# Optimization experiments

Measured on AMD Instinct MI355X. Metric: run time of the kernel, lower is better.

Reference implementation:

```python
import jax, jax.numpy as jnp
import numpy as np

B, C, H, W = 16, 384, 64, 64
NUM_POS = 48        # (7*7 - 1) offsets, origin excluded
STRIDE = 16
K = 3               # LO_kernel_size
SIGMA = 0.5         # LO_sigma


def setup_inputs() -> dict:
    key = jax.random.key(0)
    k1, k2 = jax.random.split(key)
    inp = jax.random.normal(k1, (B, C, H, W), dtype=jnp.float32)
    # init_offset: grid (iw*stride, ih*stride), skipping origin (use_origin=False)
    offs = []
    for ih in range(-3, 4):
        for iw in range(-3, 4):
            if ih == 0 and iw == 0:
                continue
            offs.append((iw * STRIDE, ih * STRIDE))
    offset = jnp.asarray(np.array(offs, dtype=np.float32))
    # small fractional perturbation so the learnable-offset gaussian path is non-trivial
    offset = offset + jax.random.uniform(k2, (NUM_POS, 2), minval=-0.45, maxval=0.45)
    return {"inp": inp, "offset": offset}


def _displace(inp, shift):
    """Integer per-channel-group spatial shift with zero padding.
    out[b,g,c,y,x] = inp[b,g,c, y - oy[g], x - ox[g]] (content moves by +offset).
    shift: [G,2] int32, (x, y) order as in the torch module.
    """
    b, c, h, w = inp.shape
    g = shift.shape[0]
    cpp = c // g
    x5 = inp.reshape(b, g, cpp, h, w)
    ox, oy = shift[:, 0], shift[:, 1]
    ys = jnp.arange(h, dtype=jnp.int32)[None, :] - oy[:, None]   # [G,H]
    xs = jnp.arange(w, dtype=jnp.int32)[None, :] - ox[:, None]   # [G,W]
    ymask = (ys >= 0) & (ys < h)
    xmask = (xs >= 0) & (xs < w)
    ysc = jnp.clip(ys, 0, h - 1)
    xsc = jnp.clip(xs, 0, w - 1)
    gth = jnp.take_along_axis(x5, ysc[None, :, None, :, None], axis=3)
    gth = jnp.take_along_axis(gth, xsc[None, :, None, None, :], axis=4)
    mask = (ymask[None, :, None, :, None] & xmask[None, :, None, None, :]).astype(inp.dtype)
    return (gth * mask).reshape(b, c, h, w)


def reference(inp, offset):
    b, c, h, w = inp.shape
    g = offset.shape[0]
    cpp = c // g
    # DisplaceCUDA uses offset.detach().round(): integer shift, no grad through it
    rnd = jax.lax.stop_gradient(jnp.round(offset))
    out = _displace(inp, rnd.astype(jnp.int32))
    # gaussian_translate: depthwise conv with gaussian kernel centered at
    # fractional part (offset - round(offset)); grads flow through this path only.
    frac = offset - rnd                                  # [G,2]
    r = jnp.arange(K, dtype=inp.dtype) - (K // 2)
    dx = r[None, None, :] + frac[:, 0, None, None]       # x varies along kernel width
    dy = r[None, :, None] + frac[:, 1, None, None]       # y varies along kernel height
    kern = jnp.exp(-(dx * dx + dy * dy) / (2.0 * SIGMA ** 2))   # [G,K,K]
    kern = kern / jnp.sum(kern, axis=(1, 2), keepdims=True)
    kern_full = jnp.repeat(kern, cpp, axis=0)[:, None]   # [C,1,K,K]
    out_LO = jax.lax.conv_general_dilated(
        out, kern_full, window_strides=(1, 1),
        padding=[(K // 2, K // 2), (K // 2, K // 2)],
        dimension_numbers=("NCHW", "OIHW", "NCHW"),
        feature_group_count=c)
    return out, out_LO
```

## Files before the change

### kernel.cpp

```cpp
#include <hip/hip_runtime.h>

#define B_   16
#define C_   384
#define H_   64
#define W_   64
#define G_   48
#define PLANE (H_ * W_)
#define SCOLS 67
#define SROWS 66
#define SELEM (SROWS * SCOLS)

__global__ __launch_bounds__(256) void displace_fused_pipe(
    const float* __restrict__ inp,
    const float* __restrict__ offset,
    float* __restrict__ out0,
    float* __restrict__ out1)
{
    __shared__ float s[2][SELEM];

    const int tid = threadIdx.x;
    const int g   = blockIdx.x % G_;
    const int b   = blockIdx.x / G_;

    const float ofx = offset[2 * g + 0];
    const float ofy = offset[2 * g + 1];
    const float rx = rintf(ofx);
    const float ry = rintf(ofy);
    const float fx = ofx - rx;
    const float fy = ofy - ry;
    const int ox = (int)rx;
    const int oy = (int)ry;

    float w[9];
    {
        float sum = 0.0f;
        #pragma unroll
        for (int i = 0; i < 3; ++i) {
            const float dy = (float)(i - 1) + fy;
            #pragma unroll
            for (int j = 0; j < 3; ++j) {
                const float dx = (float)(j - 1) + fx;
                const float v = __expf(-(dx * dx + dy * dy) * 2.0f);
                w[i * 3 + j] = v;
                sum += v;
            }
        }
        const float inv = 1.0f / sum;
        #pragma unroll
        for (int k = 0; k < 9; ++k) w[k] *= inv;
    }

    #pragma unroll
    for (int bb = 0; bb < 2; ++bb) {
        if (tid < 67) { s[bb][tid] = 0.0f; s[bb][65 * SCOLS + tid] = 0.0f; }
        if (tid < 64) { s[bb][(tid + 1) * SCOLS] = 0.0f; s[bb][(tid + 1) * SCOLS + 65] = 0.0f; }
    }

    const int lane = tid & 63;
    const int wv   = tid >> 6;
    const int sx   = lane - ox;
    const bool vx  = (unsigned)sx < (unsigned)W_;

    const float* __restrict__ base = inp + ((size_t)b * C_ + (size_t)g * 8) * PLANE;
    float* __restrict__ ob0 = out0 + ((size_t)b * C_ + (size_t)g * 8) * PLANE;
    float* __restrict__ ob1 = out1 + ((size_t)b * C_ + (size_t)g * 8) * PLANE;

    float v[16];
    #pragma unroll
    for (int k = 0; k < 16; ++k) {
        const int y  = (k << 2) + wv;
        const int sy = y - oy;
        v[k] = (vx && (unsigned)sy < (unsigned)H_) ? base[sy * W_ + sx] : 0.0f;
    }
    #pragma unroll
    for (int k = 0; k < 16; ++k) {
        const int y = (k << 2) + wv;
        s[0][(y + 1) * SCOLS + 1 + lane] = v[k];
    }
    __syncthreads();

    #pragma unroll
    for (int i = 0; i < 8; ++i) {
        if (i < 7) {
            const float* __restrict__ plane = base + (size_t)(i + 1) * PLANE;
            #pragma unroll
            for (int k = 0; k < 16; ++k) {
                const int y  = (k << 2) + wv;
                const int sy = y - oy;
                v[k] = (vx && (unsigned)sy < (unsigned)H_) ? plane[sy * W_ + sx] : 0.0f;
            }
        }

        const float* __restrict__ sb = s[i & 1];
        float* __restrict__ o0 = ob0 + (size_t)i * PLANE;
        float* __restrict__ o1 = ob1 + (size_t)i * PLANE;
        #pragma unroll
        for (int it = 0; it < 4; ++it) {
            const int pbase = it * 1024 + tid * 4;
            const int y = pbase >> 6;
            const int x = pbase & 63;
            const float* r0 = &sb[y * SCOLS + x];
            const float* r1 = r0 + SCOLS;
            const float* r2 = r1 + SCOLS;

            float p0[6], p1[6], p2[6];
            #pragma unroll
            for (int j = 0; j < 6; ++j) { p0[j] = r0[j]; p1[j] = r1[j]; p2[j] = r2[j]; }

            const float4 d0 = make_float4(p1[1], p1[2], p1[3], p1[4]);

            float a0, a1, a2, a3;
            a0 = p0[0]*w[0] + p0[1]*w[1] + p0[2]*w[2]
               + p1[0]*w[3] + p1[1]*w[4] + p1[2]*w[5]
               + p2[0]*w[6] + p2[1]*w[7] + p2[2]*w[8];
            a1 = p0[1]*w[0] + p0[2]*w[1] + p0[3]*w[2]
               + p1[1]*w[3] + p1[2]*w[4] + p1[3]*w[5]
               + p2[1]*w[6] + p2[2]*w[7] + p2[3]*w[8];
            a2 = p0[2]*w[0] + p0[3]*w[1] + p0[4]*w[2]
               + p1[2]*w[3] + p1[3]*w[4] + p1[4]*w[5]
               + p2[2]*w[6] + p2[3]*w[7] + p2[4]*w[8];
            a3 = p0[3]*w[0] + p0[4]*w[1] + p0[5]*w[2]
               + p1[3]*w[3] + p1[4]*w[4] + p1[5]*w[5]
               + p2[3]*w[6] + p2[4]*w[7] + p2[5]*w[8];

            *(float4*)(o0 + pbase) = d0;
            *(float4*)(o1 + pbase) = make_float4(a0, a1, a2, a3);
        }

        if (i < 7) {
            float* __restrict__ sw = s[(i + 1) & 1];
            #pragma unroll
            for (int k = 0; k < 16; ++k) {
                const int y = (k << 2) + wv;
                sw[(y + 1) * SCOLS + 1 + lane] = v[k];
            }
            __syncthreads();
        }
    }
}

extern "C" void kernel_launch(void* const* d_in, const int* in_sizes, int n_in,
                              void* d_out, int out_size, void* d_ws, size_t ws_size,
                              hipStream_t stream) {
    const float* inp    = (const float*)d_in[0];
    const float* offset = (const float*)d_in[1];
    float* out0 = (float*)d_out;
    float* out1 = out0 + (size_t)B_ * C_ * PLANE;
    displace_fused_pipe<<<B_ * G_, 256, 0, stream>>>(inp, offset, out0, out1);
}
```

Measured before the change: 273.5 us.

## Use separable Gaussian with column-sliding rows per thread

Factors the 3x3 Gaussian into separate x and y 1D weight sets, since exp of a sum of squares separates and the normalization factors the same way. The stencil is restructured so each thread walks 16 rows of one column, reusing horizontal partial sums across rows in registers instead of reloading 18 shared values per 4 outputs. In exchange, global stores go from float4 to scalar per-lane stores, which stay coalesced across the wavefront but issue more instructions. The kernel is likely memory bound, so the gain from fewer LDS reads and FMAs may be small.

```diff
diff --git a/kernel.cpp b/kernel.cpp
--- a/kernel.cpp
+++ b/kernel.cpp
@@ -31,28 +31,25 @@
     const int ox = (int)rx;
     const int oy = (int)ry;
 
-    float w[9];
+    float wx[3], wy[3];
     {
-        float sum = 0.0f;
+        float sxs = 0.0f, sys = 0.0f;
         #pragma unroll
-        for (int i = 0; i < 3; ++i) {
-            const float dy = (float)(i - 1) + fy;
-            #pragma unroll
-            for (int j = 0; j < 3; ++j) {
-                const float dx = (float)(j - 1) + fx;
-                const float v = __expf(-(dx * dx + dy * dy) * 2.0f);
-                w[i * 3 + j] = v;
-                sum += v;
-            }
+        for (int j = 0; j < 3; ++j) {
+            const float dx = (float)(j - 1) + fx;
+            const float dy = (float)(j - 1) + fy;
+            wx[j] = __expf(-dx * dx * 2.0f);
+            wy[j] = __expf(-dy * dy * 2.0f);
+            sxs += wx[j]; sys += wy[j];
         }
-        const float inv = 1.0f / sum;
+        const float ix = 1.0f / sxs, iy = 1.0f / sys;
         #pragma unroll
-        for (int k = 0; k < 9; ++k) w[k] *= inv;
+        for (int j = 0; j < 3; ++j) { wx[j] *= ix; wy[j] *= iy; }
     }
 
     #pragma unroll
     for (int bb = 0; bb < 2; ++bb) {
-        if (tid < 67) { s[bb][tid] = 0.0f; s[bb][65 * SCOLS + tid] = 0.0f; }
+        if (tid < 66) { s[bb][tid] = 0.0f; s[bb][65 * SCOLS + tid] = 0.0f; }
         if (tid < 64) { s[bb][(tid + 1) * SCOLS] = 0.0f; s[bb][(tid + 1) * SCOLS + 65] = 0.0f; }
     }
 
@@ -79,6 +76,9 @@
     }
     __syncthreads();
 
+    const int x  = lane;
+    const int y0 = wv << 4;
+
     #pragma unroll
     for (int i = 0; i < 8; ++i) {
         if (i < 7) {
@@ -94,37 +94,23 @@
         const float* __restrict__ sb = s[i & 1];
         float* __restrict__ o0 = ob0 + (size_t)i * PLANE;
         float* __restrict__ o1 = ob1 + (size_t)i * PLANE;
+
+        const float* rp;
+        rp = &sb[y0 * SCOLS + x];
+        float Hm = rp[0] * wx[0] + rp[1] * wx[1] + rp[2] * wx[2];
+        rp = &sb[(y0 + 1) * SCOLS + x];
+        float c0 = rp[1];
+        float Hc = rp[0] * wx[0] + c0 * wx[1] + rp[2] * wx[2];
+
         #pragma unroll
-        for (int it = 0; it < 4; ++it) {
-            const int pbase = it * 1024 + tid * 4;
-            const int y = pbase >> 6;
-            const int x = pbase & 63;
-            const float* r0 = &sb[y * SCOLS + x];
-            const float* r1 = r0 + SCOLS;
-            const float* r2 = r1 + SCOLS;
-
-            float p0[6], p1[6], p2[6];
-            #pragma unroll
-            for (int j = 0; j < 6; ++j) { p0[j] = r0[j]; p1[j] = r1[j]; p2[j] = r2[j]; }
-
-            const float4 d0 = make_float4(p1[1], p1[2], p1[3], p1[4]);
-
-            float a0, a1, a2, a3;
-            a0 = p0[0]*w[0] + p0[1]*w[1] + p0[2]*w[2]
-               + p1[0]*w[3] + p1[1]*w[4] + p1[2]*w[5]
-               + p2[0]*w[6] + p2[1]*w[7] + p2[2]*w[8];
-            a1 = p0[1]*w[0] + p0[2]*w[1] + p0[3]*w[2]
-               + p1[1]*w[3] + p1[2]*w[4] + p1[3]*w[5]
-               + p2[1]*w[6] + p2[2]*w[7] + p2[3]*w[8];
-            a2 = p0[2]*w[0] + p0[3]*w[1] + p0[4]*w[2]
-               + p1[2]*w[3] + p1[3]*w[4] + p1[4]*w[5]
-               + p2[2]*w[6] + p2[3]*w[7] + p2[4]*w[8];
-            a3 = p0[3]*w[0] + p0[4]*w[1] + p0[5]*w[2]
-               + p1[3]*w[3] + p1[4]*w[4] + p1[5]*w[5]
-               + p2[3]*w[6] + p2[4]*w[7] + p2[5]*w[8];
-
-            *(float4*)(o0 + pbase) = d0;
-            *(float4*)(o1 + pbase) = make_float4(a0, a1, a2, a3);
+        for (int r = 0; r < 16; ++r) {
+            const int row = y0 + r;
+            rp = &sb[(row + 2) * SCOLS + x];
+            const float e0 = rp[0], e1 = rp[1], e2 = rp[2];
+            const float Hp = e0 * wx[0] + e1 * wx[1] + e2 * wx[2];
+            o0[row * W_ + x] = c0;
+            o1[row * W_ + x] = Hm * wy[0] + Hc * wy[1] + Hp * wy[2];
+            Hm = Hc; Hc = Hp; c0 = e1;
         }
 
         if (i < 7) {
```

Measured after the change: 272.9 us. About the same (-0.2%).
